# Performance work log

Measured on AMD Instinct MI355X. Metric: run time of the kernel, lower is better.

Reference implementation:

```python
import jax, jax.numpy as jnp
import numpy as np

# Static config (matches init_kwargs)
D_MODEL, H, L, P = 256, 8, 4, 4
HEAD_DIM = D_MODEL // H
SPATIAL = ((76, 114), (38, 57), (19, 29), (10, 15))  # (h, w) per level
NV = sum(h * w for h, w in SPATIAL)  # 11531
B, NQ = 2, NV


def setup_inputs() -> dict:
    key = jax.random.key(0)
    ks = jax.random.split(key, 12)
    inp = {
        "query": jax.random.normal(ks[0], (B, NQ, D_MODEL), jnp.float32),
        "reference_points": jax.random.uniform(ks[1], (B, NQ, L, 2), jnp.float32),
        "value": jax.random.normal(ks[2], (B, NV, D_MODEL), jnp.float32),
        # Linear params stored as [in, out] (i.e. torch weight transposed)
        "W_off": jax.random.normal(ks[3], (D_MODEL, H * L * P * 2), jnp.float32) * 0.02,
        "b_off": jax.random.normal(ks[4], (H * L * P * 2,), jnp.float32) * 0.5,
        "W_attn": jax.random.normal(ks[5], (D_MODEL, H * L * P), jnp.float32) * 0.02,
        "b_attn": jnp.zeros((H * L * P,), jnp.float32),
        "W_val": jax.random.normal(ks[6], (D_MODEL, D_MODEL), jnp.float32) * 0.05,
        "b_val": jnp.zeros((D_MODEL,), jnp.float32),
        "W_out": jax.random.normal(ks[7], (D_MODEL, D_MODEL), jnp.float32) * 0.05,
        "b_out": jnp.zeros((D_MODEL,), jnp.float32),
    }
    return inp


def _msda(query, reference_points, value, W_off, b_off, W_attn, b_attn,
          W_val, b_val, W_out, b_out):
    Bq, Nq, C = query.shape
    D = HEAD_DIM
    # value projection -> [B, H, Nv, D]
    v = (value @ W_val + b_val).reshape(Bq, -1, H, D).transpose(0, 2, 1, 3)
    # sampling locations: ref + offset / (w, h)  -> [B, Nq, H, L, P, 2] in [0,1] coords
    off = (query @ W_off + b_off).reshape(Bq, Nq, H, L, P, 2)
    wh = jnp.array([[w, h] for h, w in SPATIAL], dtype=query.dtype)  # [L, 2]
    loc = reference_points[:, :, None, :, None, :] + off / wh[None, None, None, :, None, :]
    # attention weights softmax over L*P  -> [B, H, Nq, L, P]
    attn = jax.nn.softmax((query @ W_attn + b_attn).reshape(Bq, Nq, H, L * P), axis=-1)
    attn = attn.reshape(Bq, Nq, H, L, P).transpose(0, 2, 1, 3, 4)
    starts = np.concatenate([[0], np.cumsum([h * w for h, w in SPATIAL])]).astype(int)
    out = jnp.zeros((Bq, H, Nq, D), query.dtype)
    for l, (lh, lw) in enumerate(SPATIAL):
        feat = v[:, :, starts[l]:starts[l + 1], :]  # [B, H, lh*lw, D]
        # grid_sample align_corners=False: pixel = loc * size - 0.5
        px = loc[:, :, :, l, :, 0].transpose(0, 2, 1, 3) * lw - 0.5  # [B, H, Nq, P]
        py = loc[:, :, :, l, :, 1].transpose(0, 2, 1, 3) * lh - 0.5
        x0 = jnp.floor(px)
        y0 = jnp.floor(py)
        samp = jnp.zeros(px.shape + (D,), query.dtype)
        for dx in (0, 1):
            for dy in (0, 1):
                xi = x0 + dx
                yi = y0 + dy
                w = (1.0 - jnp.abs(px - xi)) * (1.0 - jnp.abs(py - yi))
                valid = (xi >= 0) & (xi <= lw - 1) & (yi >= 0) & (yi <= lh - 1)
                idx = (jnp.clip(yi, 0, lh - 1) * lw + jnp.clip(xi, 0, lw - 1)).astype(jnp.int32)
                g = jnp.take_along_axis(feat, idx.reshape(Bq, H, -1)[..., None], axis=2)
                g = g.reshape(Bq, H, Nq, P, D)
                samp = samp + g * jnp.where(valid, w, 0.0)[..., None]
        out = out + jnp.einsum('bhnpd,bhnp->bhnd', samp, attn[:, :, :, l, :])
    out = out.transpose(0, 2, 1, 3).reshape(Bq, Nq, C)
    return out @ W_out + b_out


def reference(query, reference_points, value, W_off, b_off, W_attn, b_attn,
              W_val, b_val, W_out, b_out):
    return _msda(query, reference_points, value, W_off, b_off, W_attn, b_attn,
                 W_val, b_val, W_out, b_out)
```

## Files before the change

kernel.cpp:

```cpp
#include <hip/hip_runtime.h>
#include <cmath>

#define B_    2
#define NQ_   11531
#define NV_   11531
#define M_    (B_ * NQ_)

typedef unsigned short u16;
typedef unsigned int   u32;
typedef __attribute__((ext_vector_type(8))) short bf16x8;
typedef __attribute__((ext_vector_type(4))) float f32x4;

__device__ __forceinline__ u16 f2bf(float f) {
    union { float f; unsigned u; } v; v.f = f;
    unsigned r = v.u + 0x7FFFu + ((v.u >> 16) & 1u);
    return (u16)(r >> 16);
}
__device__ __forceinline__ float lo_bf(u32 u) {
    union { unsigned u; float f; } v; v.u = u << 16; return v.f;
}
__device__ __forceinline__ float hi_bf(u32 u) {
    union { unsigned u; float f; } v; v.u = u & 0xFFFF0000u; return v.f;
}

__device__ __forceinline__ int sort_key(const float* __restrict__ refp, int bq) {
    const int b = bq / NQ_;
    const float2 r = *(const float2*)&refp[(size_t)bq * 8];
    int qx = (int)(r.x * 32.f); qx = min(max(qx, 0), 31);
    int qy = (int)(r.y * 32.f); qy = min(max(qy, 0), 31);
    return b * 1024 + qy * 32 + qx;
}

__global__ __launch_bounds__(256) void transpose_hist(
    const float* __restrict__ Wv, const float* __restrict__ Wo,
    const float* __restrict__ Wa, const float* __restrict__ Wu,
    const float* __restrict__ refp,
    u16* __restrict__ Tv, u16* __restrict__ Toa, u16* __restrict__ Tu,
    int* __restrict__ hist) {
    const int bid = blockIdx.x;
    if (bid >= 256) {
        const int bq = (bid - 256) * 256 + threadIdx.x;
        if (bq < M_) atomicAdd(&hist[sort_key(refp, bq)], 1);
        return;
    }
    const int z = bid >> 6;
    const float* W; u16* T; int N; int rowoff = 0;
    if (z == 0)      { W = Wv; T = Tv;  N = 256; }
    else if (z == 1) { W = Wo; T = Toa; N = 256; }
    else if (z == 2) { W = Wa; T = Toa; N = 128; rowoff = 256; }
    else             { W = Wu; T = Tu;  N = 256; }
    const int rest = bid & 63;
    const int n0 = (rest & 7) * 32, k0 = (rest >> 3) * 32;
    if (n0 >= N) return;
    __shared__ float t[32][33];
    const int c = threadIdx.x & 31, r0 = threadIdx.x >> 5;
#pragma unroll
    for (int i = 0; i < 4; ++i)
        t[r0 + i * 8][c] = W[(size_t)(k0 + r0 + i * 8) * N + n0 + c];
    __syncthreads();
#pragma unroll
    for (int i = 0; i < 4; ++i)
        T[(size_t)(rowoff + n0 + r0 + i * 8) * 256 + k0 + c] = f2bf(t[c][r0 + i * 8]);
}

__device__ void scan_block(const int* __restrict__ hist, int* __restrict__ ofs,
                           int* part) {
    const int tid = threadIdx.x;
    const int base = tid * 8;
    int loc[8]; int s = 0;
#pragma unroll
    for (int i = 0; i < 8; ++i) { loc[i] = s; s += hist[base + i]; }
    part[tid] = s;
    __syncthreads();
    for (int d = 1; d < 256; d <<= 1) {
        const int v = part[tid];
        const int u = (tid >= d) ? part[tid - d] : 0;
        __syncthreads();
        part[tid] = v + u;
        __syncthreads();
    }
    const int off = (tid > 0) ? part[tid - 1] : 0;
#pragma unroll
    for (int i = 0; i < 8; ++i) ofs[base + i] = off + loc[i];
}

__global__ __launch_bounds__(256) void scatter_kernel(const float* __restrict__ refp,
                                                      int* __restrict__ ofs,
                                                      int* __restrict__ perm) {
    const int bq = blockIdx.x * 256 + threadIdx.x;
    if (bq < M_) {
        const int pos = atomicAdd(&ofs[sort_key(refp, bq)], 1);
        perm[pos] = bq;
    }
}

template <int TN, bool ABF, int EPI>
__device__ __forceinline__ void gemm_body(const void* __restrict__ Av,
                                          const u16* __restrict__ WT,
                                          const float* __restrict__ bias,
                                          const float* __restrict__ bias2,
                                          void* __restrict__ Cv, int M,
                                          int bm, int bn,
                                          short* A_l, short* B_l) {
    constexpr int K = 256;
    const int tid = threadIdx.x;
    const int w = tid >> 6;
    const int lane = tid & 63;
    const int wr = (w >> 1) * 64;
    const int wc = (w & 1) * 64;
    const int lr = lane & 15;

    f32x4 acc[4][4] = {};

    for (int k0 = 0; k0 < K; k0 += 64) {
        if constexpr (!ABF) {
            const float* A = (const float*)Av;
#pragma unroll
            for (int i = 0; i < 8; ++i) {
                const int vid = tid + i * 256;
                const int ar = vid >> 4;
                const int ak = (vid & 15) * 4;
                const int gr = bm + ar;
                float4 av = make_float4(0.f, 0.f, 0.f, 0.f);
                if (gr < M) av = *(const float4*)&A[(size_t)gr * K + k0 + ak];
                ushort4 hv;
                hv.x = f2bf(av.x); hv.y = f2bf(av.y); hv.z = f2bf(av.z); hv.w = f2bf(av.w);
                *(ushort4*)&A_l[ar * 72 + ak] = hv;
            }
        } else {
            const u16* A = (const u16*)Av;
#pragma unroll
            for (int i = 0; i < 4; ++i) {
                const int vid = tid + i * 256;
                const int ar = vid >> 3;
                const int ak = (vid & 7) * 8;
                const int gr = bm + ar;
                uint4 hv = make_uint4(0u, 0u, 0u, 0u);
                if (gr < M) hv = *(const uint4*)&A[(size_t)gr * K + k0 + ak];
                *(uint4*)&A_l[ar * 72 + ak] = hv;
            }
        }
#pragma unroll
        for (int i = 0; i < 4; ++i) {
            const int vid = tid + i * 256;
            const int nr = vid >> 3;
            const int kk = (vid & 7) * 8;
            const uint4 wv = *(const uint4*)&WT[(size_t)(bn + nr) * K + k0 + kk];
            *(uint4*)&B_l[nr * 72 + kk] = wv;
        }
        __syncthreads();
#pragma unroll
        for (int half = 0; half < 2; ++half) {
            const int kg = half * 32 + (lane >> 4) * 8;
            bf16x8 af[4], bfr[4];
#pragma unroll
            for (int m = 0; m < 4; ++m)
                af[m] = *(const bf16x8*)&A_l[(wr + m * 16 + lr) * 72 + kg];
#pragma unroll
            for (int n = 0; n < 4; ++n)
                bfr[n] = *(const bf16x8*)&B_l[(wc + n * 16 + lr) * 72 + kg];
#pragma unroll
            for (int m = 0; m < 4; ++m)
#pragma unroll
                for (int n = 0; n < 4; ++n)
                    acc[m][n] = __builtin_amdgcn_mfma_f32_16x16x32_bf16(af[m], bfr[n], acc[m][n], 0, 0, 0);
        }
        __syncthreads();
    }

#pragma unroll
    for (int n = 0; n < 4; ++n) {
        const int gcol = bn + wc + n * 16 + lr;
        const float bv = (TN == 384 && gcol >= 256) ? bias2[gcol - 256] : bias[gcol];
#pragma unroll
        for (int m = 0; m < 4; ++m) {
            const int rbase = bm + wr + m * 16 + (lane >> 4) * 4;
#pragma unroll
            for (int j = 0; j < 4; ++j) {
                const int grow = rbase + j;
                if (grow < M) {
                    const float o = acc[m][n][j] + bv;
                    if constexpr (EPI == 2) {
                        u16* Vt = (u16*)Cv;
                        const int hh = gcol >> 5, cc = gcol & 31;
                        const size_t hb = (size_t)hh * (M_ + 2);
                        const u16 hv = f2bf(o);
                        Vt[((hb + grow) * 32 + cc) * 2] = hv;
                        if (grow > 0)
                            Vt[((hb + grow - 1) * 32 + cc) * 2 + 1] = hv;
                    } else {
                        ((float*)Cv)[(size_t)grow * TN + gcol] = o;
                    }
                }
            }
        }
    }
}

__global__ __launch_bounds__(256, 4) void gemm_stage1(
    const float* __restrict__ query, const float* __restrict__ value,
    const u16* __restrict__ WT_val, const u16* __restrict__ WT_oa,
    const float* __restrict__ b_val, const float* __restrict__ b_off,
    const float* __restrict__ b_attn,
    const int* __restrict__ hist, int* __restrict__ ofs,
    u16* __restrict__ ws_v3, float* __restrict__ ws_oa, int M, int gy) {
    __shared__ __align__(16) short A_l[128 * 72];
    __shared__ __align__(16) short B_l[128 * 72];
    int blk = blockIdx.x;
    if (blk == 5 * gy) {
        scan_block(hist, ofs, (int*)A_l);
    } else if (blk < 2 * gy) {
        gemm_body<256, false, 2>(value, WT_val, b_val, b_val, ws_v3, M,
                                 (blk >> 1) * 128, (blk & 1) * 128, A_l, B_l);
    } else {
        blk -= 2 * gy;
        gemm_body<384, false, 0>(query, WT_oa, b_off, b_attn, ws_oa, M,
                                 (blk / 3) * 128, (blk % 3) * 128, A_l, B_l);
    }
}

__global__ __launch_bounds__(256, 4) void gemm_out(
    const u16* __restrict__ samp, const u16* __restrict__ WT_out,
    const float* __restrict__ b_out, float* __restrict__ out, int M) {
    __shared__ __align__(16) short A_l[128 * 72];
    __shared__ __align__(16) short B_l[128 * 72];
    const int blk = blockIdx.x;
    gemm_body<256, true, 0>(samp, WT_out, b_out, b_out, out, M,
                            (blk >> 1) * 128, (blk & 1) * 128, A_l, B_l);
}

__global__ __launch_bounds__(512, 4) void msda_sample_v9(
    const u32* __restrict__ v3,
    const float* __restrict__ oa,
    const float* __restrict__ refp,
    const int* __restrict__ perm,
    u16* __restrict__ samp) {
    __shared__ __align__(16) float4 s_w4[1088];
    __shared__ __align__(8)  int2   s_i2[1088];
    __shared__ int s_bq[8];
    const int tid = threadIdx.x;

    const int nwg = gridDim.x;
    const int qq = nwg >> 3, rr = nwg & 7;
    const int xcd = blockIdx.x & 7, pos = blockIdx.x >> 3;
    const int wg = (xcd < rr ? xcd * (qq + 1) : rr * (qq + 1) + (xcd - rr) * qq) + pos;
    const int bq0 = wg * 8;

    if (tid < 8) {
        const int q = bq0 + tid;
        s_bq[tid] = perm[q < M_ ? q : M_ - 1];
    }
    __syncthreads();

#pragma unroll
    for (int half = 0; half < 2; ++half) {
        const int s = tid + half * 512;
        const int qi = s >> 7;
        const int rem = s & 127;
        const int sampi = rem & 15;
        const int l = sampi >> 2;
        const int h = rem >> 4;
        const int bq = s_bq[qi];
        const int b = bq / NQ_;

        const float logit = oa[(size_t)bq * 384 + 256 + rem];
        float mx = logit;
#pragma unroll
        for (int t = 8; t >= 1; t >>= 1) mx = fmaxf(mx, __shfl_xor(mx, t, 16));
        const float e = __expf(logit - mx);
        float sm = e;
#pragma unroll
        for (int t = 8; t >= 1; t >>= 1) sm += __shfl_xor(sm, t, 16);
        const float aw = e / sm;

        const float2 off = *(const float2*)&oa[(size_t)bq * 384 + rem * 2];
        const float2 rxy = *(const float2*)&refp[(size_t)bq * 8 + l * 2];
        const int lw = (l == 0) ? 114 : (l == 1) ? 57 : (l == 2) ? 29 : 15;
        const int lh = (l == 0) ? 76 : (l == 1) ? 38 : (l == 2) ? 19 : 10;
        const int st = (l == 0) ? 0 : (l == 1) ? 8664 : (l == 2) ? 10830 : 11381;
        const int base = b * NV_ + st;

        const float px = rxy.x * (float)lw + off.x - 0.5f;
        const float py = rxy.y * (float)lh + off.y - 0.5f;
        const float x0f = floorf(px), y0f = floorf(py);
        const int x0 = (int)x0f, y0 = (int)y0f;
        const float fx = px - x0f, fy = py - y0f;

        float wxlo = 0.f, wxhi = 0.f;
        if (x0 >= 0 && x0 < lw)      wxlo = 1.f - fx;
        else if (x0 == -1)           wxlo = fx;
        if (x0 >= 0 && x0 + 1 < lw)  wxhi = fx;
        const int xs = min(max(x0, 0), lw - 1);

        const float wy0 = (y0 >= 0 && y0 < lh) ? (1.f - fy) : 0.f;
        const float wy1 = (y0 + 1 >= 0 && y0 + 1 < lh) ? fy : 0.f;
        const int ys0 = min(max(y0, 0), lh - 1);
        const int ys1 = min(max(y0 + 1, 0), lh - 1);

        const int hrow = h * (M_ + 2);
        int2 iv;
        iv.x = (hrow + base + ys0 * lw + xs) << 7;
        iv.y = (hrow + base + ys1 * lw + xs) << 7;
        float4 wv;
        wv.x = aw * wxlo * wy0; wv.y = aw * wxhi * wy0;
        wv.z = aw * wxlo * wy1; wv.w = aw * wxhi * wy1;
        const int slot = (qi * 8 + h) * 17 + sampi;
        s_w4[slot] = wv;
        s_i2[slot] = iv;
    }
    __syncthreads();

    const int qi = tid >> 6;
    const int lane = tid & 63;
    const int h = lane >> 3;
    const int lcoff = (lane & 7) * 16;
    const int bq = s_bq[qi];
    const int sb = (qi * 8 + h) * 17;
    const char* vb = (const char*)v3;

    float acc0 = 0.f, acc1 = 0.f, acc2 = 0.f, acc3 = 0.f;
    float4 wc = s_w4[sb];
    {
        const int2 ic = s_i2[sb];
    }
    int2 ic = s_i2[sb];
    uint4 A0 = *(const uint4*)(vb + (u32)(ic.x + lcoff));
    uint4 A1 = *(const uint4*)(vb + (u32)(ic.y + lcoff));

#pragma unroll 2
    for (int sp = 0; sp < 16; ++sp) {
        const int nxt = (sp + 1) & 15;
        const float4 wn = s_w4[sb + nxt];
        const int2 in_ = s_i2[sb + nxt];
        const uint4 B0 = *(const uint4*)(vb + (u32)(in_.x + lcoff));
        const uint4 B1 = *(const uint4*)(vb + (u32)(in_.y + lcoff));

        acc0 = fmaf(wc.x, lo_bf(A0.x), acc0); acc0 = fmaf(wc.y, hi_bf(A0.x), acc0);
        acc0 = fmaf(wc.z, lo_bf(A1.x), acc0); acc0 = fmaf(wc.w, hi_bf(A1.x), acc0);
        acc1 = fmaf(wc.x, lo_bf(A0.y), acc1); acc1 = fmaf(wc.y, hi_bf(A0.y), acc1);
        acc1 = fmaf(wc.z, lo_bf(A1.y), acc1); acc1 = fmaf(wc.w, hi_bf(A1.y), acc1);
        acc2 = fmaf(wc.x, lo_bf(A0.z), acc2); acc2 = fmaf(wc.y, hi_bf(A0.z), acc2);
        acc2 = fmaf(wc.z, lo_bf(A1.z), acc2); acc2 = fmaf(wc.w, hi_bf(A1.z), acc2);
        acc3 = fmaf(wc.x, lo_bf(A0.w), acc3); acc3 = fmaf(wc.y, hi_bf(A0.w), acc3);
        acc3 = fmaf(wc.z, lo_bf(A1.w), acc3); acc3 = fmaf(wc.w, hi_bf(A1.w), acc3);

        wc = wn; A0 = B0; A1 = B1;
    }
    if (bq0 + qi < M_) {
        ushort4 o;
        o.x = f2bf(acc0); o.y = f2bf(acc1); o.z = f2bf(acc2); o.w = f2bf(acc3);
        *(ushort4*)&samp[(size_t)bq * 256 + (h * 32 + (lane & 7) * 4)] = o;
    }
}

extern "C" void kernel_launch(void* const* d_in, const int* in_sizes, int n_in,
                              void* d_out, int out_size, void* d_ws, size_t ws_size,
                              hipStream_t stream) {
    const float* query  = (const float*)d_in[0];
    const float* refp   = (const float*)d_in[1];
    const float* value  = (const float*)d_in[2];
    const float* W_off  = (const float*)d_in[3];
    const float* b_off  = (const float*)d_in[4];
    const float* W_attn = (const float*)d_in[5];
    const float* b_attn = (const float*)d_in[6];
    const float* W_val  = (const float*)d_in[7];
    const float* b_val  = (const float*)d_in[8];
    const float* W_out  = (const float*)d_in[9];
    const float* b_out  = (const float*)d_in[10];
    float* out = (float*)d_out;

    const int M = M_;
    u32*   ws_v3   = (u32*)d_ws;
    float* ws_oa   = (float*)(ws_v3 + (size_t)8 * (M_ + 2) * 32);
    u16*   ws_samp = (u16*)(ws_oa + (size_t)M * 384);
    u16*   WT_val  = ws_samp + (size_t)M * 256;
    u16*   WT_oa   = WT_val + 256 * 256;
    u16*   WT_out  = WT_oa + 384 * 256;
    int*   hist    = (int*)(WT_out + 256 * 256);
    int*   ofs     = hist + 2048;
    int*   perm    = ofs + 2048;

    const int gy = (M + 127) / 128;
    const int gq = (M + 255) / 256;

    hipMemsetAsync(hist, 0, 2048 * sizeof(int), stream);
    transpose_hist<<<dim3(256 + gq), 256, 0, stream>>>(W_val, W_off, W_attn, W_out,
                                                       refp, WT_val, WT_oa, WT_out, hist);
    gemm_stage1<<<dim3(5 * gy + 1), 256, 0, stream>>>(query, value, WT_val, WT_oa,
                                                      b_val, b_off, b_attn,
                                                      hist, ofs, (u16*)ws_v3, ws_oa, M, gy);
    scatter_kernel<<<dim3(gq), 256, 0, stream>>>(refp, ofs, perm);
    msda_sample_v9<<<dim3((M + 7) / 8), 512, 0, stream>>>(ws_v3, ws_oa, refp, perm, ws_samp);
    gemm_out<<<dim3(2 * gy), 256, 0, stream>>>(ws_samp, WT_out, b_out, out, M);
}
```

Before: 114.6 us.

## Move value x-pair packing from GEMM epilogue into separate coalesced repack pass

```diff
diff --git a/kernel.cpp b/kernel.cpp
--- a/kernel.cpp
+++ b/kernel.cpp
@@ -84,14 +84,35 @@
     for (int i = 0; i < 8; ++i) ofs[base + i] = off + loc[i];
 }
 
-__global__ __launch_bounds__(256) void scatter_kernel(const float* __restrict__ refp,
-                                                      int* __restrict__ ofs,
-                                                      int* __restrict__ perm) {
-    const int bq = blockIdx.x * 256 + threadIdx.x;
-    if (bq < M_) {
-        const int pos = atomicAdd(&ofs[sort_key(refp, bq)], 1);
-        perm[pos] = bq;
-    }
+__global__ __launch_bounds__(256) void repack_scatter(
+    const u16* __restrict__ ws_v, const float* __restrict__ refp,
+    int* __restrict__ ofs, int* __restrict__ perm,
+    u32* __restrict__ v3, int nsc) {
+    const int bid = blockIdx.x;
+    const int tid = threadIdx.x;
+    if (bid < nsc) {
+        const int bq = bid * 256 + tid;
+        if (bq < M_) {
+            const int pos = atomicAdd(&ofs[sort_key(refp, bq)], 1);
+            perm[pos] = bq;
+        }
+        return;
+    }
+    const int g4 = (bid - nsc) * 256 + tid;
+    if (g4 >= 8 * M_ * 8) return;
+    const int h = g4 / (M_ * 8);
+    const int rem = g4 - h * (M_ * 8);
+    const int r = rem >> 3;
+    const int c = (rem & 7) * 4;
+    const ushort4 lo = *(const ushort4*)&ws_v[(size_t)r * 256 + h * 32 + c];
+    ushort4 hi = make_ushort4(0, 0, 0, 0);
+    if (r + 1 < M_) hi = *(const ushort4*)&ws_v[(size_t)(r + 1) * 256 + h * 32 + c];
+    uint4 o;
+    o.x = (u32)lo.x | ((u32)hi.x << 16);
+    o.y = (u32)lo.y | ((u32)hi.y << 16);
+    o.z = (u32)lo.z | ((u32)hi.z << 16);
+    o.w = (u32)lo.w | ((u32)hi.w << 16);
+    *(uint4*)&v3[((size_t)h * M_ + r) * 32 + c] = o;
 }
 
 template <int TN, bool ABF, int EPI>
@@ -180,17 +201,8 @@
                 const int grow = rbase + j;
                 if (grow < M) {
                     const float o = acc[m][n][j] + bv;
-                    if constexpr (EPI == 2) {
-                        u16* Vt = (u16*)Cv;
-                        const int hh = gcol >> 5, cc = gcol & 31;
-                        const size_t hb = (size_t)hh * (M_ + 2);
-                        const u16 hv = f2bf(o);
-                        Vt[((hb + grow) * 32 + cc) * 2] = hv;
-                        if (grow > 0)
-                            Vt[((hb + grow - 1) * 32 + cc) * 2 + 1] = hv;
-                    } else {
-                        ((float*)Cv)[(size_t)grow * TN + gcol] = o;
-                    }
+                    if constexpr (EPI == 1) ((u16*)Cv)[(size_t)grow * TN + gcol] = f2bf(o);
+                    else                    ((float*)Cv)[(size_t)grow * TN + gcol] = o;
                 }
             }
         }
@@ -203,14 +215,14 @@
     const float* __restrict__ b_val, const float* __restrict__ b_off,
     const float* __restrict__ b_attn,
     const int* __restrict__ hist, int* __restrict__ ofs,
-    u16* __restrict__ ws_v3, float* __restrict__ ws_oa, int M, int gy) {
+    u16* __restrict__ ws_v, float* __restrict__ ws_oa, int M, int gy) {
     __shared__ __align__(16) short A_l[128 * 72];
     __shared__ __align__(16) short B_l[128 * 72];
     int blk = blockIdx.x;
     if (blk == 5 * gy) {
         scan_block(hist, ofs, (int*)A_l);
     } else if (blk < 2 * gy) {
-        gemm_body<256, false, 2>(value, WT_val, b_val, b_val, ws_v3, M,
+        gemm_body<256, false, 1>(value, WT_val, b_val, b_val, ws_v, M,
                                  (blk >> 1) * 128, (blk & 1) * 128, A_l, B_l);
     } else {
         blk -= 2 * gy;
@@ -229,7 +241,7 @@
                             (blk >> 1) * 128, (blk & 1) * 128, A_l, B_l);
 }
 
-__global__ __launch_bounds__(512, 4) void msda_sample_v9(
+__global__ __launch_bounds__(512, 4) void msda_sample_v10(
     const u32* __restrict__ v3,
     const float* __restrict__ oa,
     const float* __restrict__ refp,
@@ -297,7 +309,7 @@
         const int ys0 = min(max(y0, 0), lh - 1);
         const int ys1 = min(max(y0 + 1, 0), lh - 1);
 
-        const int hrow = h * (M_ + 2);
+        const int hrow = h * M_;
         int2 iv;
         iv.x = (hrow + base + ys0 * lw + xs) << 7;
         iv.y = (hrow + base + ys1 * lw + xs) << 7;
@@ -320,9 +332,6 @@
 
     float acc0 = 0.f, acc1 = 0.f, acc2 = 0.f, acc3 = 0.f;
     float4 wc = s_w4[sb];
-    {
-        const int2 ic = s_i2[sb];
-    }
     int2 ic = s_i2[sb];
     uint4 A0 = *(const uint4*)(vb + (u32)(ic.x + lcoff));
     uint4 A1 = *(const uint4*)(vb + (u32)(ic.y + lcoff));
@@ -370,10 +379,11 @@
     float* out = (float*)d_out;
 
     const int M = M_;
-    u32*   ws_v3   = (u32*)d_ws;
-    float* ws_oa   = (float*)(ws_v3 + (size_t)8 * (M_ + 2) * 32);
-    u16*   ws_samp = (u16*)(ws_oa + (size_t)M * 384);
-    u16*   WT_val  = ws_samp + (size_t)M * 256;
+    u16*   ws_v    = (u16*)d_ws;
+    u16*   ws_samp = ws_v;
+    u32*   ws_v3   = (u32*)(ws_v + (size_t)M * 256);
+    float* ws_oa   = (float*)(ws_v3 + (size_t)8 * M * 32);
+    u16*   WT_val  = (u16*)(ws_oa + (size_t)M * 384);
     u16*   WT_oa   = WT_val + 256 * 256;
     u16*   WT_out  = WT_oa + 384 * 256;
     int*   hist    = (int*)(WT_out + 256 * 256);
@@ -382,14 +392,16 @@
 
     const int gy = (M + 127) / 128;
     const int gq = (M + 255) / 256;
+    const int grep = (8 * M * 8 + 255) / 256;
 
     hipMemsetAsync(hist, 0, 2048 * sizeof(int), stream);
     transpose_hist<<<dim3(256 + gq), 256, 0, stream>>>(W_val, W_off, W_attn, W_out,
                                                        refp, WT_val, WT_oa, WT_out, hist);
     gemm_stage1<<<dim3(5 * gy + 1), 256, 0, stream>>>(query, value, WT_val, WT_oa,
                                                       b_val, b_off, b_attn,
-                                                      hist, ofs, (u16*)ws_v3, ws_oa, M, gy);
-    scatter_kernel<<<dim3(gq), 256, 0, stream>>>(refp, ofs, perm);
-    msda_sample_v9<<<dim3((M + 7) / 8), 512, 0, stream>>>(ws_v3, ws_oa, refp, perm, ws_samp);
+                                                      hist, ofs, ws_v, ws_oa, M, gy);
+    repack_scatter<<<dim3(gq + grep), 256, 0, stream>>>(ws_v, refp, ofs, perm,
+                                                        ws_v3, gq);
+    msda_sample_v10<<<dim3((M + 7) / 8), 512, 0, stream>>>(ws_v3, ws_oa, refp, perm, ws_samp);
     gemm_out<<<dim3(2 * gy), 256, 0, stream>>>(ws_samp, WT_out, b_out, out, M);
 }
```

New measurement: 115.6 us. No clear change (+0.8%).
